# Optimization experiments

Measured on AMD Instinct MI355X. Metric: run time of the kernel, lower is better.

Reference implementation:

```python
import jax, jax.numpy as jnp
import numpy as np

NUM_CLASSES = 80
NUM_KERNELS = 256
NUM_GRIDS = (40, 36, 24, 16, 12)
STRIDES = (8, 8, 16, 32, 32)
SCORE_THR = 0.1
MASK_THR = 0.5
UPDATE_THR = 0.05
NMS_PRE = 500
MAX_PER_IMG = 100
NMS_SIGMA = 2.0
ORI_H, ORI_W = 640, 960  # ratio*f_h = 4*160, 4*240 -> upsampled == ori size


def point_nms(heat, kernel=2):
    # torch: hmax = max_pool2d(heat, 2, stride=1, padding=1)[..., :-1, :-1]
    # equivalent: 2x2 window with (1,0) padding top/left, -inf init
    hmax = jax.lax.reduce_window(
        heat, -jnp.inf, jax.lax.max,
        (1, 1, kernel, kernel), (1, 1, 1, 1),
        ((0, 0), (0, 0), (1, 0), (1, 0)))
    return heat * (hmax == heat).astype(heat.dtype)


def setup_inputs() -> dict:
    key = jax.random.key(0)
    ks = jax.random.split(key, 11)
    inp = {}
    for i, g in enumerate(NUM_GRIDS):
        inp[f"cate_p{i}"] = jax.random.normal(ks[i], (1, NUM_CLASSES, g, g), jnp.float32)
        inp[f"kern_p{i}"] = jax.random.normal(ks[5 + i], (1, NUM_KERNELS, g, g), jnp.float32) * 0.05
    inp["mask_feat"] = jax.random.normal(ks[10], (1, NUM_KERNELS, 160, 240), jnp.float32)
    return inp


def _solo_post(cate_list, kern_list, mask_feat):
    # point-NMS on sigmoid scores, flatten grids, concat levels  -> [S, C]
    cate = jnp.concatenate([
        point_nms(jax.nn.sigmoid(c))[0].transpose(1, 2, 0).reshape(-1, NUM_CLASSES)
        for c in cate_list], axis=0)
    kern = jnp.concatenate([
        k[0].transpose(1, 2, 0).reshape(-1, NUM_KERNELS) for k in kern_list], axis=0)
    strides = jnp.concatenate([
        jnp.full((g * g,), float(s), jnp.float32) for g, s in zip(NUM_GRIDS, STRIDES)])

    # score threshold -> fixed-size top-k selection (jit-friendly)
    flat = jnp.where(cate > SCORE_THR, cate, 0.0).reshape(-1)  # [S*C]
    scores, flat_idx = jax.lax.top_k(flat, NMS_PRE)
    grid_idx = flat_idx // NUM_CLASSES
    labels = flat_idx % NUM_CLASSES
    valid = scores > 0.0

    # 1x1 dynamic conv == matmul over channel dim
    kp = kern[grid_idx]                                   # [N, K]
    st = strides[grid_idx]                                # [N]
    seg = jax.nn.sigmoid(jnp.einsum('nk,khw->nhw', kp, mask_feat[0]))  # [N, h, w]
    seg_masks = seg > MASK_THR
    sum_masks = seg_masks.sum((1, 2)).astype(jnp.float32)
    keep = (sum_masks > st) & valid
    seg_score = (seg * seg_masks).sum((1, 2)) / jnp.maximum(sum_masks, 1.0)
    scores = scores * seg_score * keep.astype(scores.dtype)

    # sort descending by updated scores
    order = jnp.argsort(-scores)
    scores = scores[order]
    labels = labels[order]
    seg = seg[order]
    alive = (scores > 0.0).astype(jnp.float32)
    masks_f = seg_masks[order].astype(jnp.float32) * alive[:, None, None]
    sum_m = masks_f.sum((1, 2))

    # matrix NMS (gaussian)
    mflat = masks_f.reshape(NMS_PRE, -1)
    inter = mflat @ mflat.T                               # [N, N]
    union = sum_m[:, None] + sum_m[None, :] - inter
    iou = jnp.triu(jnp.where(union > 0, inter / jnp.maximum(union, 1.0), 0.0), k=1)
    label_m = jnp.triu((labels[:, None] == labels[None, :]).astype(jnp.float32), k=1)
    decay_iou = iou * label_m
    comp_iou = decay_iou.max(axis=0)                      # per instance (column max)
    # decay[i, j] = exp(-sigma*(decay_iou[i,j]^2 - comp_iou[i]^2)); coef = min over i
    decay = jnp.exp(-NMS_SIGMA * (decay_iou ** 2 - comp_iou[:, None] ** 2))
    scores = scores * decay.min(axis=0)

    scores = scores * (scores >= UPDATE_THR).astype(scores.dtype)
    top_s, top_i = jax.lax.top_k(scores, MAX_PER_IMG)
    seg_top = seg[top_i]                                  # [M, h, w]

    # upsample to (f_h*ratio, f_w*ratio) then to ori_size (equal here), crop no-op
    up = jax.image.resize(seg_top, (MAX_PER_IMG, ORI_H, ORI_W), method='bilinear')
    up2 = jax.image.resize(up, (MAX_PER_IMG, ORI_H, ORI_W), method='bilinear')
    return up2, top_s, top_i, labels


def reference(cate_p0, cate_p1, cate_p2, cate_p3, cate_p4,
              kern_p0, kern_p1, kern_p2, kern_p3, kern_p4, mask_feat):
    up2, top_s, top_i, labels = _solo_post(
        [cate_p0, cate_p1, cate_p2, cate_p3, cate_p4],
        [kern_p0, kern_p1, kern_p2, kern_p3, kern_p4], mask_feat)
    pred_masks = up2 > MASK_THR
    return pred_masks, top_s, labels[top_i]
```

## Files before the change

### kernel.cpp

```cpp
#include <hip/hip_runtime.h>
#include <stdint.h>

#define NCLS 80
#define NKER 256
#define STOT 3872
#define NFLAT (STOT*NCLS)
#define NPRE 500
#define NPREP 512
#define MAXI 100
#define MH 160
#define MW 240
#define MP (MH*MW)
#define OH 640
#define OW 960
#define NWORD 600
#define PARTW 300

#define BN 64
#define BP 128
#define BK 64

#define WS_HIST   0u
#define WS_META   262144u
#define WS_IOU    266240u
#define WS_ZEROB  2266240u
#define WS_FLAT   2266240u
#define WS_CANDV  3505280u
#define WS_CANDI  3521664u
#define WS_SEL    3538048u
#define WS_KPT    3591296u
#define WS_MB     4115584u
#define WS_PART   6515584u
#define WS_SEG    7715584u

__device__ __forceinline__ float bf2f(unsigned short u) { return __uint_as_float(((unsigned)u) << 16); }
__device__ __forceinline__ unsigned short f2bf(float f) {
  unsigned b = __float_as_uint(f);
  return (unsigned short)((b + 0x7fffu + ((b >> 16) & 1u)) >> 16);
}
__device__ __forceinline__ unsigned fkey(float f) {
  unsigned b = __float_as_uint(f);
  return b ^ ((b & 0x80000000u) ? 0xFFFFFFFFu : 0x80000000u);
}

__global__ __launch_bounds__(256) void k_flat(
    const float* __restrict__ c0, const float* __restrict__ c1, const float* __restrict__ c2,
    const float* __restrict__ c3, const float* __restrict__ c4,
    float* __restrict__ flat, unsigned* __restrict__ hist) {
  int idx = blockIdx.x * 256 + threadIdx.x;
  if (idx >= NFLAT) return;
  int s = idx / NCLS, c = idx - s * NCLS;
  const float* base; int g, cell;
  if (s < 1600)      { base = c0; g = 40; cell = s; }
  else if (s < 2896) { base = c1; g = 36; cell = s - 1600; }
  else if (s < 3472) { base = c2; g = 24; cell = s - 2896; }
  else if (s < 3728) { base = c3; g = 16; cell = s - 3472; }
  else               { base = c4; g = 12; cell = s - 3728; }
  int i = cell / g, j = cell - i * g;
  const float* ch = base + c * g * g;
  float x = ch[i * g + j];
  float m = x;
  if (i > 0 && j > 0) m = fmaxf(m, ch[(i - 1) * g + j - 1]);
  if (i > 0)          m = fmaxf(m, ch[(i - 1) * g + j]);
  if (j > 0)          m = fmaxf(m, ch[i * g + j - 1]);
  bool pass = (x >= m) && ((double)x > -2.1972245773362196 );
  flat[idx] = pass ? x : __int_as_float(0xFF800000);
  if (pass) atomicAdd(&hist[fkey(x) >> 16], 1u);
}

__global__ void k_pivot(const unsigned* __restrict__ hist, unsigned* __restrict__ meta) {
  __shared__ unsigned csum[1024];
  int t = threadIdx.x;
  int hi = 65536 - t * 64, lo = hi - 64;
  unsigned s = 0;
  for (int b = lo; b < hi; ++b) s += hist[b];
  csum[t] = s;
  __syncthreads();
  if (t == 0) {
    unsigned cum = 0;
    for (int cch = 0; cch < 1024; ++cch) {
      if (cum + csum[cch] >= NPRE) {
        int chi = 65536 - cch * 64;
        for (int b = chi - 1; b >= chi - 64; --b) {
          if (cum + hist[b] >= NPRE) { meta[1] = (unsigned)b; return; }
          cum += hist[b];
        }
      }
      cum += csum[cch];
    }
    meta[1] = 0u;
  }
}

__global__ __launch_bounds__(256) void k_compact(
    const float* __restrict__ flat, float* __restrict__ cv, int* __restrict__ ci,
    unsigned* __restrict__ meta) {
  int idx = blockIdx.x * 256 + threadIdx.x;
  if (idx >= NFLAT) return;
  float v = flat[idx];
  if (__float_as_uint(v) == 0xFF800000u) return;
  if ((fkey(v) >> 16) >= meta[1]) {
    unsigned pos = atomicAdd(&meta[0], 1u);
    if (pos < 4096u) { cv[pos] = v; ci[pos] = idx; }
  }
}

__global__ __launch_bounds__(1024) void k_select(
    const float* __restrict__ cv, const int* __restrict__ ci, const unsigned* __restrict__ meta,
    double* __restrict__ sel_score, unsigned* __restrict__ sel_grid,
    unsigned* __restrict__ sel_label, double* __restrict__ sel_stride) {
  __shared__ float sv[4096];
  __shared__ int si[4096];
  int t = threadIdx.x;
  int n = (meta[0] < 4096u) ? (int)meta[0] : 4096;
  for (int i = t; i < 4096; i += 1024) {
    if (i < n) { sv[i] = cv[i]; si[i] = ci[i]; }
    else       { sv[i] = __int_as_float(0xFF800000); si[i] = (1 << 30) + i; }
  }
  __syncthreads();
  for (int k = 2; k <= 4096; k <<= 1)
    for (int j = k >> 1; j > 0; j >>= 1) {
      for (int i = t; i < 4096; i += 1024) {
        int ix = i ^ j;
        if (ix > i) {
          float v1 = sv[i], v2 = sv[ix]; int i1 = si[i], i2 = si[ix];
          bool b2 = (v2 > v1) || (v2 == v1 && i2 < i1);
          bool dir = (i & k) == 0;
          if (dir == b2) { sv[i] = v2; sv[ix] = v1; si[i] = i2; si[ix] = i1; }
        }
      }
      __syncthreads();
    }
  for (int i = t; i < NPREP; i += 1024) {
    if (i < NPRE && i < n) {
      int fidx = si[i];
      unsigned gi = (unsigned)fidx / NCLS;
      sel_score[i] = 1.0 / (1.0 + exp(-(double)sv[i]));
      sel_grid[i] = gi;
      sel_label[i] = (unsigned)fidx - gi * NCLS;
      sel_stride[i] = gi < 2896u ? 8.0 : (gi < 3472u ? 16.0 : 32.0);
    } else {
      sel_score[i] = 0.0; sel_grid[i] = 0u; sel_label[i] = 0u; sel_stride[i] = 1e18;
    }
  }
}

__global__ __launch_bounds__(256) void k_gather(
    const float* __restrict__ k0, const float* __restrict__ k1, const float* __restrict__ k2,
    const float* __restrict__ k3, const float* __restrict__ k4,
    const unsigned* __restrict__ sel_grid, float* __restrict__ kpT) {
  int tid = blockIdx.x * 256 + threadIdx.x;
  if (tid >= NPREP * NKER) return;
  int n = tid & (NPREP - 1);
  int k = tid >> 9;
  float v = 0.f;
  if (n < NPRE) {
    unsigned gi = sel_grid[n];
    const float* base; unsigned g, cell;
    if (gi < 1600u)      { base = k0; g = 40; cell = gi; }
    else if (gi < 2896u) { base = k1; g = 36; cell = gi - 1600u; }
    else if (gi < 3472u) { base = k2; g = 24; cell = gi - 2896u; }
    else if (gi < 3728u) { base = k3; g = 16; cell = gi - 3472u; }
    else                 { base = k4; g = 12; cell = gi - 3728u; }
    v = base[(unsigned)k * g * g + cell];
  }
  kpT[k * NPREP + n] = v;
}

__global__ __launch_bounds__(256, 3) void k_gemm(
    const float* __restrict__ kpT, const float* __restrict__ mf,
    unsigned short* __restrict__ seg, unsigned long long* __restrict__ mb,
    double* __restrict__ part) {
  __shared__ float As[BK][BN];
  __shared__ float Bs[BK][BP];
  int p0 = blockIdx.x * BP, n0 = blockIdx.y * BN;
  int tid = threadIdx.x;
  int tp = tid & 15, tn = tid >> 4;
  double acc[4][8] = {};
  for (int kc = 0; kc < NKER; kc += BK) {
    for (int q = tid; q < BK * 16; q += 256) {
      int row = q >> 4, c4 = (q & 15) << 2;
      *(float4*)&As[row][c4] = *(const float4*)&kpT[(kc + row) * NPREP + n0 + c4];
    }
    for (int q = tid; q < BK * 32; q += 256) {
      int row = q >> 5, c4 = (q & 31) << 2;
      *(float4*)&Bs[row][c4] = *(const float4*)&mf[(size_t)(kc + row) * MP + p0 + c4];
    }
    __syncthreads();
#pragma unroll 4
    for (int k = 0; k < BK; ++k) {
      float4 af = *(float4*)&As[k][tn << 2];
      float4 b0 = *(float4*)&Bs[k][tp << 2];
      float4 b1 = *(float4*)&Bs[k][64 + (tp << 2)];
      double a[4] = {af.x, af.y, af.z, af.w};
      double b[8] = {b0.x, b0.y, b0.z, b0.w, b1.x, b1.y, b1.z, b1.w};
#pragma unroll
      for (int r = 0; r < 4; ++r)
#pragma unroll
        for (int c = 0; c < 8; ++c)
          acc[r][c] = fma(a[r], b[c], acc[r][c]);
    }
    __syncthreads();
  }
  double* partL = (double*)&As[0][0];
  unsigned* nibL = (unsigned*)((char*)&As[0][0] + 8192);
  for (int r = 0; r < 4; ++r) {
    int nl = (tn << 2) + r;
    int nn = n0 + nl;
    unsigned nb = 0; double wsum = 0.0;
    unsigned short u[8];
#pragma unroll
    for (int c = 0; c < 8; ++c) {
      float z = (float)acc[r][c];
      float sf = 1.0f / (1.0f + __expf(-z));
      u[c] = f2bf(sf);
      if (acc[r][c] > 0.0) { nb |= 1u << c; wsum += (double)sf; }
    }
    if (nn < NPRE) {
      ushort4 o0; o0.x = u[0]; o0.y = u[1]; o0.z = u[2]; o0.w = u[3];
      ushort4 o1; o1.x = u[4]; o1.y = u[5]; o1.z = u[6]; o1.w = u[7];
      *(ushort4*)&seg[(size_t)nn * MP + p0 + (tp << 2)] = o0;
      *(ushort4*)&seg[(size_t)nn * MP + p0 + 64 + (tp << 2)] = o1;
    }
    partL[nl * 16 + tp] = wsum;
    nibL[nl * 16 + tp] = nb;
  }
  __syncthreads();
  if (tid < 64) {
    int nn = n0 + tid;
    if (nn < NPRE) {
      double ssum = 0.0; unsigned long long w0 = 0ull, w1 = 0ull;
#pragma unroll
      for (int c = 0; c < 16; ++c) {
        ssum += partL[tid * 16 + c];
        unsigned nb = nibL[tid * 16 + c];
        w0 |= (unsigned long long)(nb & 0xFu) << (c << 2);
        w1 |= (unsigned long long)(nb >> 4) << (c << 2);
      }
      int bx = blockIdx.x;
      part[nn * PARTW + bx] = ssum;
      mb[nn * NWORD + bx * 2] = w0;
      mb[nn * NWORD + bx * 2 + 1] = w1;
    }
  }
}

__global__ void k_masks(const unsigned long long* __restrict__ mb, const double* __restrict__ part,
                        const double* __restrict__ sel_score, const double* __restrict__ sel_stride,
                        double* __restrict__ summask, double* __restrict__ upd) {
  int n = blockIdx.x, t = threadIdx.x;
  int cnt = 0; double ws = 0.0;
  for (int j = t; j < NWORD; j += 64) cnt += __popcll(mb[n * NWORD + j]);
  for (int j = t; j < PARTW; j += 64) ws += part[n * PARTW + j];
  for (int o = 32; o > 0; o >>= 1) { cnt += __shfl_down(cnt, o); ws += __shfl_down(ws, o); }
  if (t == 0) {
    double cf = (double)cnt;
    double ss = ws / fmax(cf, 1.0);
    double raw = sel_score[n];
    bool keep = (cf > sel_stride[n]) && (raw > 0.0);
    summask[n] = cf;
    upd[n] = keep ? raw * ss : 0.0;
  }
}

__global__ __launch_bounds__(512) void k_sort(
    const double* __restrict__ upd, const unsigned* __restrict__ sel_label, const double* __restrict__ summask,
    double* __restrict__ s_score, unsigned* __restrict__ s_slot, unsigned* __restrict__ s_label2,
    double* __restrict__ s_sum, unsigned* __restrict__ s_alive) {
  __shared__ double sv[NPREP];
  __shared__ int si[NPREP];
  int t = threadIdx.x;
  sv[t] = (t < NPRE) ? upd[t] : -1.0;
  si[t] = t;
  __syncthreads();
  for (int k = 2; k <= NPREP; k <<= 1)
    for (int j = k >> 1; j > 0; j >>= 1) {
      int ix = t ^ j;
      if (ix > t) {
        double v1 = sv[t], v2 = sv[ix]; int i1 = si[t], i2 = si[ix];
        bool b2 = (v2 > v1) || (v2 == v1 && i2 < i1);
        bool dir = (t & k) == 0;
        if (dir == b2) { sv[t] = v2; sv[ix] = v1; si[t] = i2; si[ix] = i1; }
      }
      __syncthreads();
    }
  double sc = sv[t]; int slot = si[t];
  bool alive = sc > 0.0;
  s_score[t] = alive ? sc : 0.0;
  s_slot[t] = (unsigned)slot;
  s_label2[t] = sel_label[slot];
  s_sum[t] = (alive && slot < NPRE) ? summask[slot] : 0.0;
  s_alive[t] = alive ? 1u : 0u;
}

__global__ __launch_bounds__(256) void k_inter(
    const unsigned long long* __restrict__ mb, const unsigned* __restrict__ s_slot,
    const unsigned* __restrict__ s_label2, const unsigned* __restrict__ s_alive,
    const double* __restrict__ s_sum, double* __restrict__ iou) {
  int w = (blockIdx.x * 256 + threadIdx.x) >> 6;
  int lane = threadIdx.x & 63;
  if (w >= NPRE * NPRE) return;
  int i = w / NPRE, j = w - i * NPRE;
  if (i >= j) return;
  if (s_label2[i] != s_label2[j] || !s_alive[i] || !s_alive[j]) return;
  const unsigned long long* A = mb + (size_t)s_slot[i] * NWORD;
  const unsigned long long* B = mb + (size_t)s_slot[j] * NWORD;
  int c = 0;
  for (int wd = lane; wd < NWORD; wd += 64) c += __popcll(A[wd] & B[wd]);
  for (int o = 32; o > 0; o >>= 1) c += __shfl_down(c, o);
  if (lane == 0) {
    double inter = (double)c;
    double uni = s_sum[i] + s_sum[j] - inter;
    iou[i * NPRE + j] = (uni > 0.0) ? inter / fmax(uni, 1.0) : 0.0;
  }
}

__global__ __launch_bounds__(512) void k_nms(const double* __restrict__ iou,
                                             const double* __restrict__ s_score,
                                             double* __restrict__ final_) {
  __shared__ double compS[NPREP];
  int t = threadIdx.x;
  double cm = 0.0;
  if (t < NPRE)
    for (int i = 0; i < t; ++i) cm = fmax(cm, iou[i * NPRE + t]);
  compS[t] = cm;
  __syncthreads();
  if (t < NPRE) {
    double m = 0.0;
    for (int i = 0; i < t; ++i) {
      double d = iou[i * NPRE + t];
      m = fmax(m, d * d - compS[i] * compS[i]);
    }
    double f = s_score[t] * exp(-2.0 * m);
    final_[t] = (f >= 0.05) ? f : 0.0;
  } else {
    final_[t] = 0.0;
  }
}

__global__ __launch_bounds__(512) void k_top100(
    const double* __restrict__ final_, const unsigned* __restrict__ s_label2,
    const unsigned* __restrict__ s_slot, float* __restrict__ d_out, int maskN,
    unsigned* __restrict__ up_slot) {
  __shared__ double sv[NPREP];
  __shared__ int si[NPREP];
  int t = threadIdx.x;
  sv[t] = final_[t]; si[t] = t;
  __syncthreads();
  for (int k = 2; k <= NPREP; k <<= 1)
    for (int j = k >> 1; j > 0; j >>= 1) {
      int ix = t ^ j;
      if (ix > t) {
        double v1 = sv[t], v2 = sv[ix]; int i1 = si[t], i2 = si[ix];
        bool b2 = (v2 > v1) || (v2 == v1 && i2 < i1);
        bool dir = (t & k) == 0;
        if (dir == b2) { sv[t] = v2; sv[ix] = v1; si[t] = i2; si[ix] = i1; }
      }
      __syncthreads();
    }
  if (t < MAXI) {
    int pos = si[t];
    d_out[maskN + t] = (float)sv[t];
    d_out[maskN + MAXI + t] = (float)s_label2[pos];
    up_slot[t] = s_slot[pos];
  }
}

__global__ __launch_bounds__(256) void k_up(const unsigned short* __restrict__ seg,
                                            const unsigned* __restrict__ up_slot,
                                            float* __restrict__ out, int maskN) {
  int o = blockIdx.x * 256 + threadIdx.x;
  if (o >= maskN) return;
  int m = o / (OH * OW);
  int rem = o - m * (OH * OW);
  int y = rem / OW, x = rem - y * OW;
  const unsigned short* row = seg + (size_t)up_slot[m] * MP;
  float sy = y * 0.25f - 0.375f, sx = x * 0.25f - 0.375f;
  int y0 = (int)floorf(sy), x0 = (int)floorf(sx);
  float wy = sy - y0, wx = sx - x0;
  int y0c = max(y0, 0), y1c = min(y0 + 1, MH - 1);
  int x0c = max(x0, 0), x1c = min(x0 + 1, MW - 1);
  float s00 = bf2f(row[y0c * MW + x0c]), s01 = bf2f(row[y0c * MW + x1c]);
  float s10 = bf2f(row[y1c * MW + x0c]), s11 = bf2f(row[y1c * MW + x1c]);
  float v = (1.f - wy) * ((1.f - wx) * s00 + wx * s01) + wy * ((1.f - wx) * s10 + wx * s11);
  out[o] = (v > 0.5f) ? 1.f : 0.f;
}

extern "C" void kernel_launch(void* const* d_in, const int* in_sizes, int n_in,
                              void* d_out, int out_size, void* d_ws, size_t ws_size,
                              hipStream_t stream) {
  const float* c0 = (const float*)d_in[0];
  const float* k0 = (const float*)d_in[1];
  const float* c1 = (const float*)d_in[2];
  const float* k1 = (const float*)d_in[3];
  const float* c2 = (const float*)d_in[4];
  const float* k2 = (const float*)d_in[5];
  const float* c3 = (const float*)d_in[6];
  const float* k3 = (const float*)d_in[7];
  const float* c4 = (const float*)d_in[8];
  const float* k4 = (const float*)d_in[9];
  const float* mf = (const float*)d_in[10];

  char* ws = (char*)d_ws;
  unsigned* hist = (unsigned*)(ws + WS_HIST);
  unsigned* meta = (unsigned*)(ws + WS_META);
  double* iou = (double*)(ws + WS_IOU);
  float* flat = (float*)(ws + WS_FLAT);
  float* cv = (float*)(ws + WS_CANDV);
  int* ci = (int*)(ws + WS_CANDI);
  double* sel_score  = (double*)(ws + WS_SEL + 0);
  unsigned* sel_grid = (unsigned*)(ws + WS_SEL + 4096);
  unsigned* sel_label= (unsigned*)(ws + WS_SEL + 8192);
  double* sel_stride = (double*)(ws + WS_SEL + 12288);
  double* upd        = (double*)(ws + WS_SEL + 16384);
  double* summask    = (double*)(ws + WS_SEL + 20480);
  double* s_score    = (double*)(ws + WS_SEL + 24576);
  unsigned* s_slot   = (unsigned*)(ws + WS_SEL + 28672);
  unsigned* s_label2 = (unsigned*)(ws + WS_SEL + 32768);
  double* s_sum      = (double*)(ws + WS_SEL + 36864);
  unsigned* s_alive  = (unsigned*)(ws + WS_SEL + 40960);
  double* final_     = (double*)(ws + WS_SEL + 45056);
  unsigned* up_slot  = (unsigned*)(ws + WS_SEL + 49152);
  float* kpT = (float*)(ws + WS_KPT);
  unsigned long long* mb = (unsigned long long*)(ws + WS_MB);
  double* part = (double*)(ws + WS_PART);
  unsigned short* seg = (unsigned short*)(ws + WS_SEG);

  int maskN = out_size - 2 * MAXI;

  hipMemsetAsync(ws, 0, WS_ZEROB, stream);

  k_flat<<<(NFLAT + 255) / 256, 256, 0, stream>>>(c0, c1, c2, c3, c4, flat, hist);
  k_pivot<<<1, 1024, 0, stream>>>(hist, meta);
  k_compact<<<(NFLAT + 255) / 256, 256, 0, stream>>>(flat, cv, ci, meta);
  k_select<<<1, 1024, 0, stream>>>(cv, ci, meta, sel_score, sel_grid, sel_label, sel_stride);
  k_gather<<<(NPREP * NKER + 255) / 256, 256, 0, stream>>>(k0, k1, k2, k3, k4, sel_grid, kpT);
  dim3 g6(MP / BP, NPREP / BN);
  k_gemm<<<g6, 256, 0, stream>>>(kpT, mf, seg, mb, part);
  k_masks<<<NPRE, 64, 0, stream>>>(mb, part, sel_score, sel_stride, summask, upd);
  k_sort<<<1, NPREP, 0, stream>>>(upd, sel_label, summask, s_score, s_slot, s_label2, s_sum, s_alive);
  k_inter<<<(NPRE * NPRE) / 4, 256, 0, stream>>>(mb, s_slot, s_label2, s_alive, s_sum, iou);
  k_nms<<<1, NPREP, 0, stream>>>(iou, s_score, final_);
  k_top100<<<1, NPREP, 0, stream>>>(final_, s_label2, s_slot, (float*)d_out, maskN, up_slot);
  k_up<<<(maskN + 255) / 256, 256, 0, stream>>>(seg, up_slot, (float*)d_out, maskN);
}
```

Measured before the change: 724.6 us.

## Convert GEMM tiles to double in LDS, fuse NMS+top100, vectorize upsample, shrink memset

The GEMM now converts its fp32 tiles to double once when staging into LDS, halving BK to fit, so the inner loop skips the per-iteration float-to-double conversions. The IoU kernel now writes every upper-triangle entry, which lets the memset skip the IoU region, and the NMS and top-100 kernels are merged into one launch. The upsample kernel emits four output pixels per thread with fixed bilinear weights and float4 stores. The mask bit packing and seg column layout are changed to match the new thread-to-column mapping, which risks subtle ordering bugs; doubling the LDS footprint may reduce occupancy.

New measurement: 671.2 us. 1.08x faster.

```diff
diff --git a/kernel.cpp b/kernel.cpp
--- a/kernel.cpp
+++ b/kernel.cpp
@@ -18,12 +18,12 @@
 
 #define BN 64
 #define BP 128
-#define BK 64
+#define BK 32
 
 #define WS_HIST   0u
 #define WS_META   262144u
+#define WS_ZEROB  266240u
 #define WS_IOU    266240u
-#define WS_ZEROB  2266240u
 #define WS_FLAT   2266240u
 #define WS_CANDV  3505280u
 #define WS_CANDI  3521664u
@@ -171,29 +171,40 @@
     const float* __restrict__ kpT, const float* __restrict__ mf,
     unsigned short* __restrict__ seg, unsigned long long* __restrict__ mb,
     double* __restrict__ part) {
-  __shared__ float As[BK][BN];
-  __shared__ float Bs[BK][BP];
+  __shared__ double Asd[BK][BN];
+  __shared__ double Bsd[BK][BP];
   int p0 = blockIdx.x * BP, n0 = blockIdx.y * BN;
   int tid = threadIdx.x;
   int tp = tid & 15, tn = tid >> 4;
   double acc[4][8] = {};
   for (int kc = 0; kc < NKER; kc += BK) {
-    for (int q = tid; q < BK * 16; q += 256) {
-      int row = q >> 4, c4 = (q & 15) << 2;
-      *(float4*)&As[row][c4] = *(const float4*)&kpT[(kc + row) * NPREP + n0 + c4];
-    }
-    for (int q = tid; q < BK * 32; q += 256) {
-      int row = q >> 5, c4 = (q & 31) << 2;
-      *(float4*)&Bs[row][c4] = *(const float4*)&mf[(size_t)(kc + row) * MP + p0 + c4];
+#pragma unroll
+    for (int it = 0; it < 4; ++it) {
+      int q = it * 256 + tid;
+      int row = q >> 5, c2 = q & 31;
+      float2 f = *(const float2*)&kpT[(kc + row) * NPREP + n0 + c2 * 2];
+      double2 d; d.x = (double)f.x; d.y = (double)f.y;
+      *(double2*)&Asd[row][c2 * 2] = d;
+    }
+#pragma unroll
+    for (int it = 0; it < 8; ++it) {
+      int q = it * 256 + tid;
+      int row = q >> 6, c2 = q & 63;
+      float2 f = *(const float2*)&mf[(size_t)(kc + row) * MP + p0 + c2 * 2];
+      double2 d; d.x = (double)f.x; d.y = (double)f.y;
+      *(double2*)&Bsd[row][c2 * 2] = d;
     }
     __syncthreads();
 #pragma unroll 4
     for (int k = 0; k < BK; ++k) {
-      float4 af = *(float4*)&As[k][tn << 2];
-      float4 b0 = *(float4*)&Bs[k][tp << 2];
-      float4 b1 = *(float4*)&Bs[k][64 + (tp << 2)];
-      double a[4] = {af.x, af.y, af.z, af.w};
-      double b[8] = {b0.x, b0.y, b0.z, b0.w, b1.x, b1.y, b1.z, b1.w};
+      double2 a01 = *(double2*)&Asd[k][(tn << 2)];
+      double2 a23 = *(double2*)&Asd[k][(tn << 2) + 2];
+      double2 b0 = *(double2*)&Bsd[k][tp * 2];
+      double2 b1 = *(double2*)&Bsd[k][32 + tp * 2];
+      double2 b2 = *(double2*)&Bsd[k][64 + tp * 2];
+      double2 b3 = *(double2*)&Bsd[k][96 + tp * 2];
+      double a[4] = {a01.x, a01.y, a23.x, a23.y};
+      double b[8] = {b0.x, b0.y, b1.x, b1.y, b2.x, b2.y, b3.x, b3.y};
 #pragma unroll
       for (int r = 0; r < 4; ++r)
 #pragma unroll
@@ -202,8 +213,8 @@
     }
     __syncthreads();
   }
-  double* partL = (double*)&As[0][0];
-  unsigned* nibL = (unsigned*)((char*)&As[0][0] + 8192);
+  double* partL = (double*)&Asd[0][0];
+  unsigned* nibL = (unsigned*)((char*)&Asd[0][0] + 8192);
   for (int r = 0; r < 4; ++r) {
     int nl = (tn << 2) + r;
     int nn = n0 + nl;
@@ -217,10 +228,11 @@
       if (acc[r][c] > 0.0) { nb |= 1u << c; wsum += (double)sf; }
     }
     if (nn < NPRE) {
-      ushort4 o0; o0.x = u[0]; o0.y = u[1]; o0.z = u[2]; o0.w = u[3];
-      ushort4 o1; o1.x = u[4]; o1.y = u[5]; o1.z = u[6]; o1.w = u[7];
-      *(ushort4*)&seg[(size_t)nn * MP + p0 + (tp << 2)] = o0;
-      *(ushort4*)&seg[(size_t)nn * MP + p0 + 64 + (tp << 2)] = o1;
+#pragma unroll
+      for (int g = 0; g < 4; ++g) {
+        ushort2 o; o.x = u[2 * g]; o.y = u[2 * g + 1];
+        *(ushort2*)&seg[(size_t)nn * MP + p0 + g * 32 + tp * 2] = o;
+      }
     }
     partL[nl * 16 + tp] = wsum;
     nibL[nl * 16 + tp] = nb;
@@ -233,9 +245,9 @@
 #pragma unroll
       for (int c = 0; c < 16; ++c) {
         ssum += partL[tid * 16 + c];
-        unsigned nb = nibL[tid * 16 + c];
-        w0 |= (unsigned long long)(nb & 0xFu) << (c << 2);
-        w1 |= (unsigned long long)(nb >> 4) << (c << 2);
+        unsigned long long nb = (unsigned long long)nibL[tid * 16 + c];
+        w0 |= ((nb      & 3ull) << (c * 2)) | (((nb >> 2) & 3ull) << (32 + c * 2));
+        w1 |= (((nb >> 4) & 3ull) << (c * 2)) | (((nb >> 6) & 3ull) << (32 + c * 2));
       }
       int bx = blockIdx.x;
       part[nn * PARTW + bx] = ssum;
@@ -302,50 +314,44 @@
   if (w >= NPRE * NPRE) return;
   int i = w / NPRE, j = w - i * NPRE;
   if (i >= j) return;
-  if (s_label2[i] != s_label2[j] || !s_alive[i] || !s_alive[j]) return;
-  const unsigned long long* A = mb + (size_t)s_slot[i] * NWORD;
-  const unsigned long long* B = mb + (size_t)s_slot[j] * NWORD;
-  int c = 0;
-  for (int wd = lane; wd < NWORD; wd += 64) c += __popcll(A[wd] & B[wd]);
-  for (int o = 32; o > 0; o >>= 1) c += __shfl_down(c, o);
-  if (lane == 0) {
+  double val = 0.0;
+  if (s_label2[i] == s_label2[j] && s_alive[i] && s_alive[j]) {
+    const unsigned long long* A = mb + (size_t)s_slot[i] * NWORD;
+    const unsigned long long* B = mb + (size_t)s_slot[j] * NWORD;
+    int c = 0;
+    for (int wd = lane; wd < NWORD; wd += 64) c += __popcll(A[wd] & B[wd]);
+    for (int o = 32; o > 0; o >>= 1) c += __shfl_down(c, o);
     double inter = (double)c;
     double uni = s_sum[i] + s_sum[j] - inter;
-    iou[i * NPRE + j] = (uni > 0.0) ? inter / fmax(uni, 1.0) : 0.0;
-  }
-}
-
-__global__ __launch_bounds__(512) void k_nms(const double* __restrict__ iou,
-                                             const double* __restrict__ s_score,
-                                             double* __restrict__ final_) {
+    val = (uni > 0.0) ? inter / fmax(uni, 1.0) : 0.0;
+  }
+  if (lane == 0) iou[i * NPRE + j] = val;
+}
+
+__global__ __launch_bounds__(512) void k_nms_top(
+    const double* __restrict__ iou, const double* __restrict__ s_score,
+    const unsigned* __restrict__ s_label2, const unsigned* __restrict__ s_slot,
+    float* __restrict__ d_out, int maskN, unsigned* __restrict__ up_slot) {
   __shared__ double compS[NPREP];
+  __shared__ double sv[NPREP];
+  __shared__ int si[NPREP];
   int t = threadIdx.x;
   double cm = 0.0;
   if (t < NPRE)
     for (int i = 0; i < t; ++i) cm = fmax(cm, iou[i * NPRE + t]);
   compS[t] = cm;
   __syncthreads();
+  double f = 0.0;
   if (t < NPRE) {
     double m = 0.0;
     for (int i = 0; i < t; ++i) {
       double d = iou[i * NPRE + t];
       m = fmax(m, d * d - compS[i] * compS[i]);
     }
-    double f = s_score[t] * exp(-2.0 * m);
-    final_[t] = (f >= 0.05) ? f : 0.0;
-  } else {
-    final_[t] = 0.0;
-  }
-}
-
-__global__ __launch_bounds__(512) void k_top100(
-    const double* __restrict__ final_, const unsigned* __restrict__ s_label2,
-    const unsigned* __restrict__ s_slot, float* __restrict__ d_out, int maskN,
-    unsigned* __restrict__ up_slot) {
-  __shared__ double sv[NPREP];
-  __shared__ int si[NPREP];
-  int t = threadIdx.x;
-  sv[t] = final_[t]; si[t] = t;
+    f = s_score[t] * exp(-2.0 * m);
+    if (f < 0.05) f = 0.0;
+  }
+  sv[t] = f; si[t] = t;
   __syncthreads();
   for (int k = 2; k <= NPREP; k <<= 1)
     for (int j = k >> 1; j > 0; j >>= 1) {
@@ -369,21 +375,34 @@
 __global__ __launch_bounds__(256) void k_up(const unsigned short* __restrict__ seg,
                                             const unsigned* __restrict__ up_slot,
                                             float* __restrict__ out, int maskN) {
-  int o = blockIdx.x * 256 + threadIdx.x;
-  if (o >= maskN) return;
-  int m = o / (OH * OW);
-  int rem = o - m * (OH * OW);
-  int y = rem / OW, x = rem - y * OW;
+  int o4 = (blockIdx.x * 256 + threadIdx.x) * 4;
+  if (o4 >= maskN) return;
+  int m = o4 / (OH * OW);
+  int rem = o4 - m * (OH * OW);
+  int y = rem / OW;
+  int x = rem - y * OW;
+  int a = x >> 2;
   const unsigned short* row = seg + (size_t)up_slot[m] * MP;
-  float sy = y * 0.25f - 0.375f, sx = x * 0.25f - 0.375f;
-  int y0 = (int)floorf(sy), x0 = (int)floorf(sx);
-  float wy = sy - y0, wx = sx - x0;
+  float sy = y * 0.25f - 0.375f;
+  int y0 = (int)floorf(sy);
+  float wy = sy - y0;
   int y0c = max(y0, 0), y1c = min(y0 + 1, MH - 1);
-  int x0c = max(x0, 0), x1c = min(x0 + 1, MW - 1);
-  float s00 = bf2f(row[y0c * MW + x0c]), s01 = bf2f(row[y0c * MW + x1c]);
-  float s10 = bf2f(row[y1c * MW + x0c]), s11 = bf2f(row[y1c * MW + x1c]);
-  float v = (1.f - wy) * ((1.f - wx) * s00 + wx * s01) + wy * ((1.f - wx) * s10 + wx * s11);
-  out[o] = (v > 0.5f) ? 1.f : 0.f;
+  const unsigned short* r0 = row + y0c * MW;
+  const unsigned short* r1 = row + y1c * MW;
+  int t0 = max(a - 1, 0), t1 = a, t2 = min(a + 1, MW - 1);
+  float T0 = bf2f(r0[t0]), T1 = bf2f(r0[t1]), T2 = bf2f(r0[t2]);
+  float B0 = bf2f(r1[t0]), B1 = bf2f(r1[t1]), B2 = bf2f(r1[t2]);
+  float iwy = 1.f - wy;
+  float4 o;
+  o.x = iwy * (0.375f * T0 + 0.625f * T1) + wy * (0.375f * B0 + 0.625f * B1);
+  o.y = iwy * (0.125f * T0 + 0.875f * T1) + wy * (0.125f * B0 + 0.875f * B1);
+  o.z = iwy * (0.875f * T1 + 0.125f * T2) + wy * (0.875f * B1 + 0.125f * B2);
+  o.w = iwy * (0.625f * T1 + 0.375f * T2) + wy * (0.625f * B1 + 0.375f * B2);
+  o.x = (o.x > 0.5f) ? 1.f : 0.f;
+  o.y = (o.y > 0.5f) ? 1.f : 0.f;
+  o.z = (o.z > 0.5f) ? 1.f : 0.f;
+  o.w = (o.w > 0.5f) ? 1.f : 0.f;
+  *(float4*)&out[o4] = o;
 }
 
 extern "C" void kernel_launch(void* const* d_in, const int* in_sizes, int n_in,
@@ -419,7 +438,6 @@
   unsigned* s_label2 = (unsigned*)(ws + WS_SEL + 32768);
   double* s_sum      = (double*)(ws + WS_SEL + 36864);
   unsigned* s_alive  = (unsigned*)(ws + WS_SEL + 40960);
-  double* final_     = (double*)(ws + WS_SEL + 45056);
   unsigned* up_slot  = (unsigned*)(ws + WS_SEL + 49152);
   float* kpT = (float*)(ws + WS_KPT);
   unsigned long long* mb = (unsigned long long*)(ws + WS_MB);
@@ -440,7 +458,6 @@
   k_masks<<<NPRE, 64, 0, stream>>>(mb, part, sel_score, sel_stride, summask, upd);
   k_sort<<<1, NPREP, 0, stream>>>(upd, sel_label, summask, s_score, s_slot, s_label2, s_sum, s_alive);
   k_inter<<<(NPRE * NPRE) / 4, 256, 0, stream>>>(mb, s_slot, s_label2, s_alive, s_sum, iou);
-  k_nms<<<1, NPREP, 0, stream>>>(iou, s_score, final_);
-  k_top100<<<1, NPREP, 0, stream>>>(final_, s_label2, s_slot, (float*)d_out, maskN, up_slot);
-  k_up<<<(maskN + 255) / 256, 256, 0, stream>>>(seg, up_slot, (float*)d_out, maskN);
-}
+  k_nms_top<<<1, NPREP, 0, stream>>>(iou, s_score, s_label2, s_slot, (float*)d_out, maskN, up_slot);
+  k_up<<<(maskN / 4 + 255) / 256, 256, 0, stream>>>(seg, up_slot, (float*)d_out, maskN);
+}
```
